# Kernel optimization log

Hardware: AMD Instinct MI355X
Metric: run time of the kernel (lower is better)

## Reference

```python
import jax, jax.numpy as jnp
import numpy as np

QUERY_DIM = 512
INNER_DIM = 2 * QUERY_DIM  # 1024
CROSS_DIM = 512


def setup_inputs() -> dict:
    key = jax.random.key(0)
    k1, k2, k3, k4, k5, k6, k7 = jax.random.split(key, 7)
    B, N1, N2 = 8, 2048, 2048
    S1 = jax.random.normal(k1, (B, N1, CROSS_DIM), dtype=jnp.float32)
    S2 = jax.random.normal(k2, (B, N2, QUERY_DIM), dtype=jnp.float32)
    # Linear weights stored as [in, out] (pre-transposed vs torch's [out, in])
    sq = 1.0 / np.sqrt(QUERY_DIM)
    sc = 1.0 / np.sqrt(CROSS_DIM)
    si = 1.0 / np.sqrt(INNER_DIM)
    Wq = jax.random.uniform(k3, (QUERY_DIM, INNER_DIM), jnp.float32, -sq, sq)
    Wk = jax.random.uniform(k4, (CROSS_DIM, INNER_DIM), jnp.float32, -sc, sc)
    Wv = jax.random.uniform(k5, (CROSS_DIM, INNER_DIM), jnp.float32, -sc, sc)
    Wo = jax.random.uniform(k6, (INNER_DIM, QUERY_DIM), jnp.float32, -si, si)
    bo = jax.random.uniform(k7, (QUERY_DIM,), jnp.float32, -si, si)
    return {"S1": S1, "S2": S2, "Wq": Wq, "Wk": Wk, "Wv": Wv, "Wo": Wo, "bo": bo}


def reference(S1, S2, Wq, Wk, Wv, Wo, bo):
    # softmax((Wq S2)(Wk S1)^T) (Wv S1), then output projection. NOTE: no 1/sqrt(d) scaling.
    query = jnp.einsum('bnd,de->bne', S2, Wq)   # [B, N2, inner]
    key_ = jnp.einsum('bmd,de->bme', S1, Wk)    # [B, N1, inner]
    value = jnp.einsum('bmd,de->bme', S1, Wv)   # [B, N1, inner]
    scores = jnp.einsum('bne,bme->bnm', query, key_)  # [B, N2, N1]
    attn = jax.nn.softmax(scores, axis=-1)
    masked = jnp.einsum('bnm,bme->bne', attn, value)  # [B, N2, inner]
    out = jnp.einsum('bne,ed->bnd', masked, Wo) + bo  # [B, N2, query_dim]
    return out
```

## Files before the change

kernel.cpp:

```cpp
#include <hip/hip_runtime.h>


typedef _Float16 h_t;
typedef _Float16 h8 __attribute__((ext_vector_type(8)));
typedef _Float16 h4 __attribute__((ext_vector_type(4)));
typedef float f4 __attribute__((ext_vector_type(4)));

#define MFMA16(a, b, c) __builtin_amdgcn_mfma_f32_16x16x32_f16(a, b, c, 0, 0, 0)

typedef const __attribute__((address_space(1))) void* gas_t;
typedef __attribute__((address_space(3))) void* las_t;

__device__ __forceinline__ void gl2lds16(const void* g, void* l) {
    __builtin_amdgcn_global_load_lds((gas_t)g, (las_t)l, 16, 0, 0);
}

__global__ __launch_bounds__(256) void k_prep(const float* __restrict__ S1,
                                              const float* __restrict__ S2,
                                              const float* __restrict__ Wq,
                                              const float* __restrict__ Wk,
                                              const float* __restrict__ Wv,
                                              const float* __restrict__ Wo,
                                              h_t* __restrict__ S1h,
                                              h_t* __restrict__ S2h,
                                              h_t* __restrict__ Wqh,
                                              h_t* __restrict__ Wkh,
                                              h_t* __restrict__ Wvh,
                                              h_t* __restrict__ Wot) {
    __shared__ float tile[32][33];
    long bid = blockIdx.x;
    if (bid < 17920) {
        long i = bid * 256 + threadIdx.x;
        const long n = 2097152;
        const long wn = 131072;
        const float* src;
        h_t* dst;
        long off;
        if (i < n) { src = S1; dst = S1h; off = i; }
        else if (i < 2 * n) { src = S2; dst = S2h; off = i - n; }
        else if (i < 2 * n + wn) { src = Wq; dst = Wqh; off = i - 2 * n; }
        else if (i < 2 * n + 2 * wn) { src = Wk; dst = Wkh; off = i - 2 * n - wn; }
        else { src = Wv; dst = Wvh; off = i - 2 * n - 2 * wn; }
        float4 v = *((const float4*)src + off);
        h4 h = {(h_t)v.x, (h_t)v.y, (h_t)v.z, (h_t)v.w};
        *((h4*)dst + off) = h;
    } else {
        int tid = (int)(bid - 17920);
        const int K = 1024, N = 512;
        int nb = (tid & 15) * 32, kb = (tid >> 4) * 32;
        int x = threadIdx.x & 31, y = threadIdx.x >> 5;
#pragma unroll
        for (int j = 0; j < 4; j++)
            tile[y + j * 8][x] = Wo[(size_t)(kb + y + j * 8) * N + nb + x];
        __syncthreads();
#pragma unroll
        for (int j = 0; j < 4; j++)
            Wot[(size_t)(nb + y + j * 8) * K + kb + x] = (h_t)tile[x][y + j * 8];
    }
}

__global__ __launch_bounds__(256) void k_wpre(const h_t* __restrict__ Wqh,
                                              const h_t* __restrict__ Wkh,
                                              const h_t* __restrict__ Wot,
                                              const h_t* __restrict__ Wvh,
                                              h_t* __restrict__ Wkq,
                                              h_t* __restrict__ Wvot) {
    __shared__ h_t As[128 * 64];
    __shared__ h_t Bs[128 * 64];
    int t = threadIdx.x, w = t >> 6, lane = t & 63;
    int q16 = lane >> 4, l16 = lane & 15;
    int id = blockIdx.x;
    const h_t* A;
    const h_t* Bt;
    h_t* C;
    float oscale;
    if (id < 16) { A = Wkh; Bt = Wqh; C = Wkq; oscale = 1.44269504f; }
    else { id -= 16; A = Wot; Bt = Wvh; C = Wvot; oscale = 1.0f; }
    size_t m0 = (size_t)(id >> 2) * 128, n0 = (size_t)(id & 3) * 128;
    const int K = 1024, N = 512;
    int wr = (w >> 1) * 64, wc = (w & 1) * 64;
    f4 acc[4][4] = {};

    for (int k0 = 0; k0 < K; k0 += 64) {
#pragma unroll
        for (int j = 0; j < 4; j++) {
            int q = w * 4 + j;
            int row = q * 8 + (lane >> 3);
            int ks = (((lane & 7) ^ (row & 7)) << 3);
            gl2lds16(A + (m0 + row) * K + k0 + ks, &As[q * 512]);
            gl2lds16(Bt + (n0 + row) * K + k0 + ks, &Bs[q * 512]);
        }
        __syncthreads();
#pragma unroll
        for (int ks = 0; ks < 2; ks++) {
            h8 av[4], bv[4];
#pragma unroll
            for (int i = 0; i < 4; i++) {
                int row = wr + i * 16 + l16;
                int ch = ks * 4 + q16;
                av[i] = *(const h8*)&As[row * 64 + ((ch ^ (row & 7)) << 3)];
            }
#pragma unroll
            for (int j = 0; j < 4; j++) {
                int row = wc + j * 16 + l16;
                int ch = ks * 4 + q16;
                bv[j] = *(const h8*)&Bs[row * 64 + ((ch ^ (row & 7)) << 3)];
            }
#pragma unroll
            for (int i = 0; i < 4; i++)
#pragma unroll
                for (int j = 0; j < 4; j++)
                    acc[i][j] = MFMA16(av[i], bv[j], acc[i][j]);
        }
        __syncthreads();
    }
#pragma unroll
    for (int i = 0; i < 4; i++) {
        size_t r0 = m0 + wr + i * 16 + q16 * 4;
#pragma unroll
        for (int j = 0; j < 4; j++) {
            size_t c = n0 + wc + j * 16 + l16;
#pragma unroll
            for (int r = 0; r < 4; r++)
                C[(r0 + r) * N + c] = (h_t)(acc[i][j][r] * oscale);
        }
    }
}

__global__ __launch_bounds__(256) void k_proj2(const h_t* __restrict__ S2h,
                                               const h_t* __restrict__ S1h,
                                               const h_t* __restrict__ Wkq,
                                               const h_t* __restrict__ Wvot,
                                               const float* __restrict__ bo,
                                               h_t* __restrict__ T,
                                               h_t* __restrict__ Vt) {
    __shared__ h_t smem[2][16384];
    int t = threadIdx.x, w = t >> 6, lane = t & 63;
    int q16 = lane >> 4, l16 = lane & 15;
    int id = blockIdx.x;
    int mode = id >> 9;
    id &= 511;
    const h_t* A = mode ? S1h : S2h;
    const h_t* Bt = mode ? Wvot : Wkq;
    size_t m0 = (size_t)(id >> 2) * 128, n0 = (size_t)(id & 3) * 128;
    int wr = (w >> 1) * 64, wc = (w & 1) * 64;
    f4 acc[4][4] = {};

    auto STAGE = [&](int k0_, int bsel) {
#pragma unroll
        for (int j = 0; j < 4; j++) {
            int q = w * 4 + j;
            int row = q * 8 + (lane >> 3);
            int ks = (((lane & 7) ^ (row & 7)) << 3);
            gl2lds16(A + (m0 + row) * 512 + k0_ + ks, &smem[bsel][q * 512]);
            gl2lds16(Bt + (n0 + row) * 512 + k0_ + ks, &smem[bsel][8192 + q * 512]);
        }
    };

    STAGE(0, 0);
    int cur = 0;
#pragma unroll 1
    for (int it = 0; it < 8; it++) {
        if (it < 7) {
            STAGE((it + 1) * 64, cur ^ 1);
            asm volatile("s_waitcnt vmcnt(8)" ::: "memory");
        } else {
            asm volatile("s_waitcnt vmcnt(0)" ::: "memory");
        }
        __builtin_amdgcn_s_barrier();
        asm volatile("" ::: "memory");
        const h_t* As = &smem[cur][0];
        const h_t* Bs = &smem[cur][8192];
#pragma unroll
        for (int ks = 0; ks < 2; ks++) {
            h8 av[4], bv[4];
#pragma unroll
            for (int i = 0; i < 4; i++) {
                int row = wr + i * 16 + l16;
                int ch = ks * 4 + q16;
                av[i] = *(const h8*)&As[row * 64 + ((ch ^ (row & 7)) << 3)];
            }
#pragma unroll
            for (int j = 0; j < 4; j++) {
                int row = wc + j * 16 + l16;
                int ch = ks * 4 + q16;
                bv[j] = *(const h8*)&Bs[row * 64 + ((ch ^ (row & 7)) << 3)];
            }
#pragma unroll
            for (int i = 0; i < 4; i++)
#pragma unroll
                for (int j = 0; j < 4; j++)
                    acc[i][j] = MFMA16(av[i], bv[j], acc[i][j]);
        }
        asm volatile("" ::: "memory");
        __builtin_amdgcn_s_barrier();
        cur ^= 1;
    }
    if (mode == 0) {
#pragma unroll
        for (int i = 0; i < 4; i++) {
            size_t r0 = m0 + wr + i * 16 + q16 * 4;
#pragma unroll
            for (int j = 0; j < 4; j++) {
                size_t c = n0 + wc + j * 16 + l16;
#pragma unroll
                for (int r = 0; r < 4; r++)
                    T[(r0 + r) * 512 + c] = (h_t)acc[i][j][r];
            }
        }
    } else {
#pragma unroll
        for (int i = 0; i < 4; i++) {
            size_t gm = m0 + wr + i * 16 + q16 * 4;
            size_t b = gm >> 11;
            size_t n = gm & 2047;
#pragma unroll
            for (int j = 0; j < 4; j++) {
                size_t d = n0 + wc + j * 16 + l16;
                float bias = bo[d];
                h4 hv = {(h_t)(acc[i][j][0] + bias), (h_t)(acc[i][j][1] + bias),
                         (h_t)(acc[i][j][2] + bias), (h_t)(acc[i][j][3] + bias)};
                *(h4*)&Vt[(b * 512 + d) * 2048 + n] = hv;
            }
        }
    }
}

__global__ __launch_bounds__(256) void k_qk(const h_t* __restrict__ T,
                                            const h_t* __restrict__ S1h,
                                            h_t* __restrict__ P,
                                            float2* __restrict__ Mkt) {
    __shared__ h_t smem[2][16384];
    __shared__ float pmx[2][128], psm[2][128];
    h_t* Ps = &smem[0][0];
    int t = threadIdx.x, w = t >> 6, lane = t & 63;
    int q16 = lane >> 4, l16 = lane & 15;
    int qt = blockIdx.x, kt = blockIdx.y, b = blockIdx.z;
    const h_t* A = S1h + ((size_t)b * 2048 + kt * 128) * 512;
    const h_t* Bt = T + ((size_t)b * 2048 + qt * 128) * 512;
    int wr = (w >> 1) * 64, wc = (w & 1) * 64;
    f4 acc[4][4] = {};

    auto STAGE = [&](int k0_, int bsel) {
#pragma unroll
        for (int j = 0; j < 4; j++) {
            int q = w * 4 + j;
            int row = q * 8 + (lane >> 3);
            int ks = (((lane & 7) ^ (row & 7)) << 3);
            gl2lds16(A + (size_t)row * 512 + k0_ + ks, &smem[bsel][q * 512]);
            gl2lds16(Bt + (size_t)row * 512 + k0_ + ks, &smem[bsel][8192 + q * 512]);
        }
    };

    STAGE(0, 0);
    int cur = 0;
#pragma unroll 1
    for (int it = 0; it < 8; it++) {
        if (it < 7) {
            STAGE((it + 1) * 64, cur ^ 1);
            asm volatile("s_waitcnt vmcnt(8)" ::: "memory");
        } else {
            asm volatile("s_waitcnt vmcnt(0)" ::: "memory");
        }
        __builtin_amdgcn_s_barrier();
        asm volatile("" ::: "memory");
        const h_t* As = &smem[cur][0];
        const h_t* Bs = &smem[cur][8192];
#pragma unroll
        for (int ks = 0; ks < 2; ks++) {
            h8 av[4], bv[4];
#pragma unroll
            for (int i = 0; i < 4; i++) {
                int row = wr + i * 16 + l16;
                int ch = ks * 4 + q16;
                av[i] = *(const h8*)&As[row * 64 + ((ch ^ (row & 7)) << 3)];
            }
#pragma unroll
            for (int j = 0; j < 4; j++) {
                int row = wc + j * 16 + l16;
                int ch = ks * 4 + q16;
                bv[j] = *(const h8*)&Bs[row * 64 + ((ch ^ (row & 7)) << 3)];
            }
#pragma unroll
            for (int i = 0; i < 4; i++)
#pragma unroll
                for (int j = 0; j < 4; j++)
                    acc[i][j] = MFMA16(av[i], bv[j], acc[i][j]);
        }
        asm volatile("" ::: "memory");
        __builtin_amdgcn_s_barrier();
        cur ^= 1;
    }
    float lm[4], ls[4], sc[4];
#pragma unroll
    for (int j = 0; j < 4; j++) {
        float m = acc[0][j][0];
#pragma unroll
        for (int i = 0; i < 4; i++)
#pragma unroll
            for (int r = 0; r < 4; r++) m = fmaxf(m, acc[i][j][r]);
        lm[j] = m;
    }
#pragma unroll
    for (int msk = 16; msk <= 32; msk <<= 1)
#pragma unroll
        for (int j = 0; j < 4; j++)
            lm[j] = fmaxf(lm[j], __shfl_xor(lm[j], msk, 64));
#pragma unroll
    for (int j = 0; j < 4; j++) {
        float s = 0.f;
#pragma unroll
        for (int i = 0; i < 4; i++)
#pragma unroll
            for (int r = 0; r < 4; r++) {
                float e = exp2f(acc[i][j][r] - lm[j]);
                acc[i][j][r] = e;
                s += e;
            }
        ls[j] = s;
    }
#pragma unroll
    for (int msk = 16; msk <= 32; msk <<= 1)
#pragma unroll
        for (int j = 0; j < 4; j++) ls[j] += __shfl_xor(ls[j], msk, 64);
    if (q16 == 0) {
#pragma unroll
        for (int j = 0; j < 4; j++) {
            pmx[w >> 1][wc + j * 16 + l16] = lm[j];
            psm[w >> 1][wc + j * 16 + l16] = ls[j];
        }
    }
    __syncthreads();
#pragma unroll
    for (int j = 0; j < 4; j++) {
        int row = wc + j * 16 + l16;
        float om = pmx[(w >> 1) ^ 1][row];
        float os = psm[(w >> 1) ^ 1][row];
        float M = fmaxf(lm[j], om);
        float s = exp2f(lm[j] - M);
        float L = ls[j] * s + os * exp2f(om - M);
        sc[j] = s;
        if ((w >> 1) == 0 && q16 == 0)
            Mkt[((size_t)b * 16 + kt) * 2048 + qt * 128 + row] = make_float2(M, L);
    }
#pragma unroll
    for (int j = 0; j < 4; j++)
#pragma unroll
        for (int i = 0; i < 4; i++) {
            h4 hv = {(h_t)(acc[i][j][0] * sc[j]), (h_t)(acc[i][j][1] * sc[j]),
                     (h_t)(acc[i][j][2] * sc[j]), (h_t)(acc[i][j][3] * sc[j])};
            *(h4*)&Ps[(wc + j * 16 + l16) * 136 + wr + i * 16 + q16 * 4] = hv;
        }
    __syncthreads();
    size_t Pbase = ((size_t)b * 2048 + qt * 128) * 2048 + (size_t)kt * 128;
#pragma unroll
    for (int p = 0; p < 8; p++) {
        int row = p * 16 + (t >> 4);
        int c8 = (t & 15) * 8;
        *(h8*)(P + Pbase + (size_t)row * 2048 + c8) = *(const h8*)&Ps[row * 136 + c8];
    }
}

__global__ __launch_bounds__(256) void k_pv(const h_t* __restrict__ P,
                                            const h_t* __restrict__ Vt,
                                            const float2* __restrict__ Mkt,
                                            float* __restrict__ Out) {
    __shared__ h_t As[128 * 64];
    __shared__ h_t Bs[2][128 * 64];
    __shared__ h_t dks[16][128];
    __shared__ float linv[128];
    int t = threadIdx.x, w = t >> 6, lane = t & 63;
    int q16 = lane >> 4, l16 = lane & 15;
    int rt = blockIdx.x, dt = blockIdx.y, b = blockIdx.z;
    int rg = w >> 1, dg = w & 1;
    if (t < 128) {
        float2 v[16];
        float m = -1e30f;
#pragma unroll
        for (int kt = 0; kt < 16; kt++) {
            v[kt] = Mkt[((size_t)b * 16 + kt) * 2048 + rt * 128 + t];
            m = fmaxf(m, v[kt].x);
        }
        float l = 0.f;
#pragma unroll
        for (int kt = 0; kt < 16; kt++) {
            float d = exp2f(v[kt].x - m);
            l += v[kt].y * d;
            dks[kt][t] = (h_t)d;
        }
        linv[t] = 1.f / l;
    }
    __syncthreads();

    const h_t* Pb = P + ((size_t)b * 2048 + rt * 128) * 2048;
    const h_t* Vb = Vt + ((size_t)b * 512 + dt * 128) * 2048;
    int srow = t >> 3, soct = t & 7;
    f4 acc[4][4] = {};
    h8 prA[4], prB[4];

    auto VSTAGE = [&](int k0_, int bsel) {
#pragma unroll
        for (int j = 0; j < 4; j++) {
            int q = w * 4 + j;
            int row = q * 8 + (lane >> 3);
            int ks = (((lane & 7) ^ (row & 7)) << 3);
            gl2lds16(Vb + (size_t)row * 2048 + k0_ + ks, &Bs[bsel][q * 512]);
        }
    };
    auto ASTORE = [&](h8* pr, int kt_) {
#pragma unroll
        for (int p = 0; p < 4; p++) {
            int r_ = p * 32 + srow;
            h_t dh = dks[kt_][r_];
            h8 dv = {dh, dh, dh, dh, dh, dh, dh, dh};
            h8 v = pr[p] * dv;
            *(h8*)&As[r_ * 64 + ((soct ^ (r_ & 7)) << 3)] = v;
        }
    };
    auto MM = [&](const h_t* Bsc) {
#pragma unroll
        for (int ks = 0; ks < 2; ks++) {
            int ch = ks * 4 + q16;
            h8 av[4], bv[4];
#pragma unroll
            for (int i = 0; i < 4; i++) {
                int row = rg * 64 + i * 16 + l16;
                av[i] = *(const h8*)&As[row * 64 + ((ch ^ (row & 7)) << 3)];
            }
#pragma unroll
            for (int j = 0; j < 4; j++) {
                int dr = dg * 64 + j * 16 + l16;
                bv[j] = *(const h8*)&Bsc[dr * 64 + ((ch ^ (dr & 7)) << 3)];
            }
#pragma unroll
            for (int i = 0; i < 4; i++)
#pragma unroll
                for (int j = 0; j < 4; j++)
                    acc[i][j] = MFMA16(av[i], bv[j], acc[i][j]);
        }
    };

#pragma unroll
    for (int p = 0; p < 4; p++)
        prA[p] = *(const h8*)(Pb + (size_t)(p * 32 + srow) * 2048 + soct * 8);
    VSTAGE(0, 0);

#pragma unroll 1
    for (int it2 = 0; it2 < 16; it2++) {
        int k0 = it2 * 128;
#pragma unroll
        for (int p = 0; p < 4; p++)
            prB[p] = *(const h8*)(Pb + (size_t)(p * 32 + srow) * 2048 + k0 + 64 + soct * 8);
        VSTAGE(k0 + 64, 1);
        asm volatile("s_waitcnt vmcnt(8)" ::: "memory");
        ASTORE(prA, k0 >> 7);
        asm volatile("s_waitcnt lgkmcnt(0)" ::: "memory");
        __builtin_amdgcn_s_barrier();
        asm volatile("" ::: "memory");
        MM(&Bs[0][0]);
        asm volatile("" ::: "memory");
        __builtin_amdgcn_s_barrier();
        if (it2 < 15) {
#pragma unroll
            for (int p = 0; p < 4; p++)
                prA[p] = *(const h8*)(Pb + (size_t)(p * 32 + srow) * 2048 + k0 + 128 + soct * 8);
            VSTAGE(k0 + 128, 0);
            asm volatile("s_waitcnt vmcnt(8)" ::: "memory");
        } else {
            asm volatile("s_waitcnt vmcnt(0)" ::: "memory");
        }
        ASTORE(prB, (k0 + 64) >> 7);
        asm volatile("s_waitcnt lgkmcnt(0)" ::: "memory");
        __builtin_amdgcn_s_barrier();
        asm volatile("" ::: "memory");
        MM(&Bs[1][0]);
        asm volatile("" ::: "memory");
        __builtin_amdgcn_s_barrier();
    }
#pragma unroll
    for (int i = 0; i < 4; i++)
#pragma unroll
        for (int rr = 0; rr < 4; rr++) {
            int row = rg * 64 + i * 16 + q16 * 4 + rr;
            float lv = linv[row];
#pragma unroll
            for (int j = 0; j < 4; j++) {
                int d = dt * 128 + dg * 64 + j * 16 + l16;
                Out[((size_t)b * 2048 + rt * 128 + row) * 512 + d] =
                    acc[i][rr >= 0 ? j : j][rr] * lv;
            }
        }
}

extern "C" void kernel_launch(void* const* d_in, const int* in_sizes, int n_in,
                              void* d_out, int out_size, void* d_ws, size_t ws_size,
                              hipStream_t stream) {
    const float* S1 = (const float*)d_in[0];
    const float* S2 = (const float*)d_in[1];
    const float* Wq = (const float*)d_in[2];
    const float* Wk = (const float*)d_in[3];
    const float* Wv = (const float*)d_in[4];
    const float* Wo = (const float*)d_in[5];
    const float* bo = (const float*)d_in[6];
    float* Out = (float*)d_out;

    char* ws = (char*)d_ws;
    h_t* S1h  = (h_t*)(ws);
    h_t* T    = (h_t*)(ws + 16777216);
    h_t* Vt   = (h_t*)(ws + 33554432);
    h_t* P    = (h_t*)(ws + 50331648);
    float2* Mkt = (float2*)(ws + 117440512);
    h_t* S2h  = (h_t*)(ws + 50331648);
    h_t* Wqh  = (h_t*)(ws + 67108864);
    h_t* Wkh  = (h_t*)(ws + 68157440);
    h_t* Wvh  = (h_t*)(ws + 69206016);
    h_t* Wot  = (h_t*)(ws + 70254592);
    h_t* Wkq  = (h_t*)(ws + 71303168);
    h_t* Wvot = (h_t*)(ws + 71827456);

    k_prep<<<18432, 256, 0, stream>>>(S1, S2, Wq, Wk, Wv, Wo,
                                      S1h, S2h, Wqh, Wkh, Wvh, Wot);
    k_wpre<<<32, 256, 0, stream>>>(Wqh, Wkh, Wot, Wvh, Wkq, Wvot);
    k_proj2<<<1024, 256, 0, stream>>>(S2h, S1h, Wkq, Wvot, bo, T, Vt);
    k_qk<<<dim3(16, 16, 8), 256, 0, stream>>>(T, S1h, P, Mkt);
    k_pv<<<dim3(16, 4, 8), 256, 0, stream>>>(P, Vt, Mkt, Out);
}
```

Baseline: 277.2 us.

## Enlarge QK score tile to 256x256 with 512-thread blocks

The QK^T kernel now computes a 256x256 score tile per block with 8 waves, each holding a 128x64 accumulator, instead of 128x128 tiles with 4 waves. Each block reuses its operand tiles across more outputs, which halves global/LDS operand traffic per score and halves the number of partial softmax stats per row. The P writeback is split into two rounds through LDS, and the PV kernel's partial-max merge is adjusted to 8 key tiles. The cost is higher register pressure (128 accumulator floats per lane), more LDS per block and fewer blocks in the grid.

```diff
diff --git a/kernel.cpp b/kernel.cpp
--- a/kernel.cpp
+++ b/kernel.cpp
@@ -226,20 +226,21 @@
     }
 }
 
-__global__ __launch_bounds__(256) void k_qk(const h_t* __restrict__ T,
-                                            const h_t* __restrict__ S1h,
-                                            h_t* __restrict__ P,
-                                            float2* __restrict__ Mkt) {
-    __shared__ h_t smem[2][16384];
-    __shared__ float pmx[2][128], psm[2][128];
+__global__ __launch_bounds__(512, 2) void k_qk(const h_t* __restrict__ T,
+                                               const h_t* __restrict__ S1h,
+                                               h_t* __restrict__ P,
+                                               float2* __restrict__ Mkt) {
+    __shared__ h_t smem[2][32768];
     h_t* Ps = &smem[0][0];
+    float* pmx = (float*)((char*)&smem[0][0] + 121856);
+    float* psm = (float*)((char*)&smem[0][0] + 123904);
     int t = threadIdx.x, w = t >> 6, lane = t & 63;
     int q16 = lane >> 4, l16 = lane & 15;
+    int wr = w >> 2, wc = w & 3;
     int qt = blockIdx.x, kt = blockIdx.y, b = blockIdx.z;
-    const h_t* A = S1h + ((size_t)b * 2048 + kt * 128) * 512;
-    const h_t* Bt = T + ((size_t)b * 2048 + qt * 128) * 512;
-    int wr = (w >> 1) * 64, wc = (w & 1) * 64;
-    f4 acc[4][4] = {};
+    const h_t* A = S1h + ((size_t)b * 2048 + kt * 256) * 512;
+    const h_t* Bt = T + ((size_t)b * 2048 + qt * 256) * 512;
+    f4 acc[8][4] = {};
 
     auto STAGE = [&](int k0_, int bsel) {
 #pragma unroll
@@ -248,7 +249,7 @@
             int row = q * 8 + (lane >> 3);
             int ks = (((lane & 7) ^ (row & 7)) << 3);
             gl2lds16(A + (size_t)row * 512 + k0_ + ks, &smem[bsel][q * 512]);
-            gl2lds16(Bt + (size_t)row * 512 + k0_ + ks, &smem[bsel][8192 + q * 512]);
+            gl2lds16(Bt + (size_t)row * 512 + k0_ + ks, &smem[bsel][16384 + q * 512]);
         }
     };
 
@@ -265,24 +266,23 @@
         __builtin_amdgcn_s_barrier();
         asm volatile("" ::: "memory");
         const h_t* As = &smem[cur][0];
-        const h_t* Bs = &smem[cur][8192];
+        const h_t* Bs = &smem[cur][16384];
 #pragma unroll
         for (int ks = 0; ks < 2; ks++) {
-            h8 av[4], bv[4];
-#pragma unroll
-            for (int i = 0; i < 4; i++) {
-                int row = wr + i * 16 + l16;
-                int ch = ks * 4 + q16;
+            int ch = ks * 4 + q16;
+            h8 av[8], bv[4];
+#pragma unroll
+            for (int i = 0; i < 8; i++) {
+                int row = wr * 128 + i * 16 + l16;
                 av[i] = *(const h8*)&As[row * 64 + ((ch ^ (row & 7)) << 3)];
             }
 #pragma unroll
             for (int j = 0; j < 4; j++) {
-                int row = wc + j * 16 + l16;
-                int ch = ks * 4 + q16;
+                int row = wc * 64 + j * 16 + l16;
                 bv[j] = *(const h8*)&Bs[row * 64 + ((ch ^ (row & 7)) << 3)];
             }
 #pragma unroll
-            for (int i = 0; i < 4; i++)
+            for (int i = 0; i < 8; i++)
 #pragma unroll
                 for (int j = 0; j < 4; j++)
                     acc[i][j] = MFMA16(av[i], bv[j], acc[i][j]);
@@ -296,7 +296,7 @@
     for (int j = 0; j < 4; j++) {
         float m = acc[0][j][0];
 #pragma unroll
-        for (int i = 0; i < 4; i++)
+        for (int i = 0; i < 8; i++)
 #pragma unroll
             for (int r = 0; r < 4; r++) m = fmaxf(m, acc[i][j][r]);
         lm[j] = m;
@@ -310,7 +310,7 @@
     for (int j = 0; j < 4; j++) {
         float s = 0.f;
 #pragma unroll
-        for (int i = 0; i < 4; i++)
+        for (int i = 0; i < 8; i++)
 #pragma unroll
             for (int r = 0; r < 4; r++) {
                 float e = exp2f(acc[i][j][r] - lm[j]);
@@ -326,38 +326,46 @@
     if (q16 == 0) {
 #pragma unroll
         for (int j = 0; j < 4; j++) {
-            pmx[w >> 1][wc + j * 16 + l16] = lm[j];
-            psm[w >> 1][wc + j * 16 + l16] = ls[j];
+            pmx[wr * 256 + wc * 64 + j * 16 + l16] = lm[j];
+            psm[wr * 256 + wc * 64 + j * 16 + l16] = ls[j];
         }
     }
     __syncthreads();
 #pragma unroll
     for (int j = 0; j < 4; j++) {
-        int row = wc + j * 16 + l16;
-        float om = pmx[(w >> 1) ^ 1][row];
-        float os = psm[(w >> 1) ^ 1][row];
+        int row = wc * 64 + j * 16 + l16;
+        float om = pmx[(wr ^ 1) * 256 + row];
+        float os = psm[(wr ^ 1) * 256 + row];
         float M = fmaxf(lm[j], om);
         float s = exp2f(lm[j] - M);
         float L = ls[j] * s + os * exp2f(om - M);
         sc[j] = s;
-        if ((w >> 1) == 0 && q16 == 0)
-            Mkt[((size_t)b * 16 + kt) * 2048 + qt * 128 + row] = make_float2(M, L);
-    }
-#pragma unroll
-    for (int j = 0; j < 4; j++)
-#pragma unroll
-        for (int i = 0; i < 4; i++) {
-            h4 hv = {(h_t)(acc[i][j][0] * sc[j]), (h_t)(acc[i][j][1] * sc[j]),
-                     (h_t)(acc[i][j][2] * sc[j]), (h_t)(acc[i][j][3] * sc[j])};
-            *(h4*)&Ps[(wc + j * 16 + l16) * 136 + wr + i * 16 + q16 * 4] = hv;
-        }
-    __syncthreads();
-    size_t Pbase = ((size_t)b * 2048 + qt * 128) * 2048 + (size_t)kt * 128;
-#pragma unroll
-    for (int p = 0; p < 8; p++) {
-        int row = p * 16 + (t >> 4);
-        int c8 = (t & 15) * 8;
-        *(h8*)(P + Pbase + (size_t)row * 2048 + c8) = *(const h8*)&Ps[row * 136 + c8];
+        if (wr == 0 && q16 == 0)
+            Mkt[((size_t)b * 8 + kt) * 2048 + qt * 256 + row] = make_float2(M, L);
+    }
+    size_t Pbase0 = ((size_t)b * 2048 + qt * 256) * 2048 + (size_t)kt * 256;
+#pragma unroll
+    for (int rnd = 0; rnd < 2; rnd++) {
+        __syncthreads();
+        if ((wc >> 1) == rnd) {
+            int rloc = (wc & 1) * 64;
+#pragma unroll
+            for (int j = 0; j < 4; j++)
+#pragma unroll
+                for (int i = 0; i < 8; i++) {
+                    h4 hv = {(h_t)(acc[i][j][0] * sc[j]), (h_t)(acc[i][j][1] * sc[j]),
+                             (h_t)(acc[i][j][2] * sc[j]), (h_t)(acc[i][j][3] * sc[j])};
+                    *(h4*)&Ps[(rloc + j * 16 + l16) * 264 + wr * 128 + i * 16 + q16 * 4] = hv;
+                }
+        }
+        __syncthreads();
+        size_t Pbase = Pbase0 + (size_t)rnd * 128 * 2048;
+#pragma unroll
+        for (int p = 0; p < 8; p++) {
+            int row = p * 16 + (t >> 5);
+            int c8 = (t & 31) * 8;
+            *(h8*)(P + Pbase + (size_t)row * 2048 + c8) = *(const h8*)&Ps[row * 264 + c8];
+        }
     }
 }
 
@@ -367,23 +375,23 @@
                                             float* __restrict__ Out) {
     __shared__ h_t As[128 * 64];
     __shared__ h_t Bs[2][128 * 64];
-    __shared__ h_t dks[16][128];
+    __shared__ h_t dks[8][128];
     __shared__ float linv[128];
     int t = threadIdx.x, w = t >> 6, lane = t & 63;
     int q16 = lane >> 4, l16 = lane & 15;
     int rt = blockIdx.x, dt = blockIdx.y, b = blockIdx.z;
     int rg = w >> 1, dg = w & 1;
     if (t < 128) {
-        float2 v[16];
+        float2 v[8];
         float m = -1e30f;
 #pragma unroll
-        for (int kt = 0; kt < 16; kt++) {
-            v[kt] = Mkt[((size_t)b * 16 + kt) * 2048 + rt * 128 + t];
+        for (int kt = 0; kt < 8; kt++) {
+            v[kt] = Mkt[((size_t)b * 8 + kt) * 2048 + rt * 128 + t];
             m = fmaxf(m, v[kt].x);
         }
         float l = 0.f;
 #pragma unroll
-        for (int kt = 0; kt < 16; kt++) {
+        for (int kt = 0; kt < 8; kt++) {
             float d = exp2f(v[kt].x - m);
             l += v[kt].y * d;
             dks[kt][t] = (h_t)d;
@@ -453,7 +461,7 @@
             prB[p] = *(const h8*)(Pb + (size_t)(p * 32 + srow) * 2048 + k0 + 64 + soct * 8);
         VSTAGE(k0 + 64, 1);
         asm volatile("s_waitcnt vmcnt(8)" ::: "memory");
-        ASTORE(prA, k0 >> 7);
+        ASTORE(prA, k0 >> 8);
         asm volatile("s_waitcnt lgkmcnt(0)" ::: "memory");
         __builtin_amdgcn_s_barrier();
         asm volatile("" ::: "memory");
@@ -469,7 +477,7 @@
         } else {
             asm volatile("s_waitcnt vmcnt(0)" ::: "memory");
         }
-        ASTORE(prB, (k0 + 64) >> 7);
+        ASTORE(prB, (k0 + 64) >> 8);
         asm volatile("s_waitcnt lgkmcnt(0)" ::: "memory");
         __builtin_amdgcn_s_barrier();
         asm volatile("" ::: "memory");
@@ -487,7 +495,7 @@
             for (int j = 0; j < 4; j++) {
                 int d = dt * 128 + dg * 64 + j * 16 + l16;
                 Out[((size_t)b * 2048 + rt * 128 + row) * 512 + d] =
-                    acc[i][rr >= 0 ? j : j][rr] * lv;
+                    acc[i][j][rr] * lv;
             }
         }
 }
@@ -522,6 +530,6 @@
                                       S1h, S2h, Wqh, Wkh, Wvh, Wot);
     k_wpre<<<32, 256, 0, stream>>>(Wqh, Wkh, Wot, Wvh, Wkq, Wvot);
     k_proj2<<<1024, 256, 0, stream>>>(S2h, S1h, Wkq, Wvot, bo, T, Vt);
-    k_qk<<<dim3(16, 16, 8), 256, 0, stream>>>(T, S1h, P, Mkt);
+    k_qk<<<dim3(8, 8, 8), 512, 0, stream>>>(T, S1h, P, Mkt);
     k_pv<<<dim3(16, 4, 8), 256, 0, stream>>>(P, Vt, Mkt, Out);
 }
```

After: 276.1 us. Within noise of the previous version (-0.4%).
